# Optimization experiments

Hardware: AMD Instinct MI355X
Metric: run time of the kernel (lower is better)

## Reference

```python
import jax, jax.numpy as jnp
import numpy as np

B, S, D, H = 4, 2048, 1024, 16
DH = D // H  # head dim == module's 'scale'


def setup_inputs() -> dict:
    key = jax.random.key(0)
    ks = jax.random.split(key, 9)
    std = 1.0 / np.sqrt(D)
    return {
        "x": jax.random.normal(ks[0], (B, S, D), dtype=jnp.float32),
        "Wq": jax.random.normal(ks[1], (D, D), dtype=jnp.float32) * std,
        "bq": jax.random.normal(ks[2], (D,), dtype=jnp.float32) * std,
        "Wk": jax.random.normal(ks[3], (D, D), dtype=jnp.float32) * std,
        "bk": jax.random.normal(ks[4], (D,), dtype=jnp.float32) * std,
        "Wv": jax.random.normal(ks[5], (D, D), dtype=jnp.float32) * std,
        "bv": jax.random.normal(ks[6], (D,), dtype=jnp.float32) * std,
        "Wo": jax.random.normal(ks[7], (D, D), dtype=jnp.float32) * std,
        "bo": jax.random.normal(ks[8], (D,), dtype=jnp.float32) * std,
    }


def reference(x, Wq, bq, Wk, bk, Wv, bv, Wo, bo):
    b, s, d = x.shape
    # torch Linear: y = x @ W.T + b
    q = (x @ Wq.T + bq).reshape(b, s, H, DH).transpose(0, 2, 1, 3)  # [B,H,S,Dh]
    k = (x @ Wk.T + bk).reshape(b, s, H, DH).transpose(0, 2, 1, 3)
    v = (x @ Wv.T + bv).reshape(b, s, H, DH).transpose(0, 2, 1, 3)
    # scaled dot-product with causal mask (prefill: Tq == Tk, empty cache)
    scores = jnp.einsum("bhqd,bhkd->bhqk", q, k) / jnp.sqrt(
        jnp.asarray(DH, dtype=jnp.float32))
    causal = jnp.tril(jnp.ones((s, s), dtype=bool))  # [S,S]
    scores = jnp.where(causal, scores, jnp.asarray(-1e9, dtype=scores.dtype))
    attn = jax.nn.softmax(scores, axis=-1)
    out = jnp.einsum("bhqk,bhkd->bhqd", attn, v)  # [B,H,S,Dh]
    out = out.transpose(0, 2, 1, 3).reshape(b, s, d)
    return out @ Wo.T + bo
```

## Files before the change

### kernel.cpp

```cpp
#include <hip/hip_runtime.h>
#include <hip/hip_bf16.h>
#include <stdint.h>

#define NB 4
#define NS 2048
#define ND 1024
#define NH 16
#define NDH 64
#define NM (NB*NS)

typedef __attribute__((ext_vector_type(8))) short bf16x8;
typedef __attribute__((ext_vector_type(4))) float f32x4;
typedef __attribute__((ext_vector_type(16))) float f32x16;
typedef __attribute__((ext_vector_type(8))) unsigned short u16x8;

static __device__ __forceinline__ unsigned short f2bf(float f) {
  union { float f; unsigned u; } v; v.f = f;
  return (unsigned short)((v.u + 0x7FFFu + ((v.u >> 16) & 1u)) >> 16);
}

static __device__ __forceinline__ void gload_lds16(const void* g, void* l) {
  __builtin_amdgcn_global_load_lds(
      (__attribute__((address_space(1))) unsigned int*)(uintptr_t)g,
      (__attribute__((address_space(3))) unsigned int*)(uintptr_t)(size_t)(l),
      16, 0, 0);
}

static __device__ __forceinline__ unsigned cvtpk(float lo, float hi) {
  unsigned r;
  asm("v_cvt_pk_bf16_f32 %0, %1, %2" : "=v"(r) : "v"(lo), "v"(hi));
  return r;
}
static __device__ __forceinline__ void plswap(unsigned &a, unsigned &b) {
  asm("v_permlane32_swap_b32 %0, %1" : "+v"(a), "+v"(b));
}

__global__ void k_cvt(const float* __restrict__ src, unsigned short* __restrict__ dst, int n8) {
  int i = blockIdx.x * blockDim.x + threadIdx.x;
  if (i >= n8) return;
  const float4* s = (const float4*)src + (size_t)i * 2;
  float4 a = s[0], b = s[1];
  u16x8 o;
  o[0]=f2bf(a.x); o[1]=f2bf(a.y); o[2]=f2bf(a.z); o[3]=f2bf(a.w);
  o[4]=f2bf(b.x); o[5]=f2bf(b.y); o[6]=f2bf(b.z); o[7]=f2bf(b.w);
  *((u16x8*)dst + i) = o;
}

__global__ void k_cvtw(const float* __restrict__ s0, const float* __restrict__ s1,
                       const float* __restrict__ s2, const float* __restrict__ s3,
                       unsigned short* __restrict__ d0, unsigned short* __restrict__ d1,
                       unsigned short* __restrict__ d2, unsigned short* __restrict__ d3) {
  constexpr int NG = ND*ND/8;
  int i = blockIdx.x * blockDim.x + threadIdx.x;
  const int m = i / NG, j = i - m*NG;
  const float* src = m==0 ? s0 : (m==1 ? s1 : (m==2 ? s2 : s3));
  unsigned short* dst = m==0 ? d0 : (m==1 ? d1 : (m==2 ? d2 : d3));
  const float4* s = (const float4*)src + (size_t)j * 2;
  float4 a = s[0], b = s[1];
  u16x8 o;
  o[0]=f2bf(a.x); o[1]=f2bf(a.y); o[2]=f2bf(a.z); o[3]=f2bf(a.w);
  o[4]=f2bf(b.x); o[5]=f2bf(b.y); o[6]=f2bf(b.z); o[7]=f2bf(b.w);
  *((u16x8*)dst + j) = o;
}

__global__ __launch_bounds__(256)
void k_gemm_qkv(const unsigned short* __restrict__ A,
                const unsigned short* __restrict__ Wqp, const unsigned short* __restrict__ Wkp,
                const unsigned short* __restrict__ Wvp,
                const float* __restrict__ bqp, const float* __restrict__ bkp,
                const float* __restrict__ bvp,
                unsigned short* __restrict__ Qo, unsigned short* __restrict__ Ko,
                unsigned short* __restrict__ Vto, float qscale)
{
  constexpr int K = ND, BK = 32;
  __shared__ unsigned short Alds[2][128*BK];
  __shared__ unsigned short Blds[2][128*BK];
  const int bcf = blockIdx.x;
  const int mat = bcf >> 3, bc = bcf & 7;
  const unsigned short* W = mat==0 ? Wqp : (mat==1 ? Wkp : Wvp);
  const float* bias = mat==0 ? bqp : (mat==1 ? bkp : bvp);
  const float scale = mat==0 ? qscale : 1.0f;

  const int tid = threadIdx.x;
  const int wid = tid >> 6, lane = tid & 63;
  const int g = lane >> 4, lr = lane & 15;
  const int br = blockIdx.y;
  const int wr = (wid >> 1) << 6, wc = (wid & 1) << 6;

  f32x4 acc[4][4];
  #pragma unroll
  for (int m=0;m<4;m++)
    #pragma unroll
    for (int n=0;n<4;n++) acc[m][n] = f32x4{0.f,0.f,0.f,0.f};

  const unsigned short* Ab = A + (size_t)br*128*K;
  const unsigned short* Wb = W + (size_t)bc*128*K;
  const int r0 = tid >> 2, c0 = (tid & 3) * 8;
  const int r1 = (256 + tid) >> 2;

  auto stage = [&](int b, int k0) {
    gload_lds16(Ab + (size_t)r0*K + k0 + c0, &Alds[b][tid*8]);
    gload_lds16(Ab + (size_t)r1*K + k0 + c0, &Alds[b][(256+tid)*8]);
    gload_lds16(Wb + (size_t)r0*K + k0 + c0, &Blds[b][tid*8]);
    gload_lds16(Wb + (size_t)r1*K + k0 + c0, &Blds[b][(256+tid)*8]);
  };

  stage(0, 0);
  __syncthreads();
  int cur = 0;
  for (int k0 = 0; k0 < K; k0 += BK) {
    if (k0 + BK < K) stage(cur ^ 1, k0 + BK);
    bf16x8 af[4], bfr[4];
    #pragma unroll
    for (int m=0;m<4;m++) af[m]  = *(const bf16x8*)&Alds[cur][(wr + m*16 + lr)*BK + g*8];
    #pragma unroll
    for (int n=0;n<4;n++) bfr[n] = *(const bf16x8*)&Blds[cur][(wc + n*16 + lr)*BK + g*8];
    __builtin_amdgcn_s_setprio(1);
    #pragma unroll
    for (int m=0;m<4;m++)
      #pragma unroll
      for (int n=0;n<4;n++)
        acc[m][n] = __builtin_amdgcn_mfma_f32_16x16x32_bf16(af[m], bfr[n], acc[m][n], 0, 0, 0);
    __builtin_amdgcn_s_setprio(0);
    __syncthreads();
    cur ^= 1;
  }

  #pragma unroll
  for (int m=0;m<4;m++) {
    const int rbase = br*128 + wr + m*16 + g*4;
    #pragma unroll
    for (int n=0;n<4;n++) {
      const int col = bc*128 + wc + n*16 + lr;
      const float bv = bias[col];
      #pragma unroll
      for (int j=0;j<4;j++) {
        const int row = rbase + j;
        const float val = (acc[m][n][j] + bv) * scale;
        const int b = row >> 11, s = row & (NS-1), h = col >> 6, dh = col & 63;
        if (mat == 2)
          Vto[(((size_t)b*NH + h)*NDH + dh)*NS + s] = f2bf(val);
        else
          (mat==0 ? Qo : Ko)[(((size_t)b*NH + h)*NS + s)*NDH + dh] = f2bf(val);
      }
    }
  }
}

__global__ __launch_bounds__(256)
void k_gemm_o(const unsigned short* __restrict__ A,
              const unsigned short* __restrict__ W,
              const float* __restrict__ bias,
              float* __restrict__ outp)
{
  constexpr int K = ND, BK = 32;
  __shared__ unsigned short Alds[2][128*BK];
  __shared__ unsigned short Blds[2][128*BK];
  const int tid = threadIdx.x;
  const int wid = tid >> 6, lane = tid & 63;
  const int g = lane >> 4, lr = lane & 15;
  const int bc = blockIdx.x, br = blockIdx.y;
  const int wr = (wid >> 1) << 6, wc = (wid & 1) << 6;

  f32x4 acc[4][4];
  #pragma unroll
  for (int m=0;m<4;m++)
    #pragma unroll
    for (int n=0;n<4;n++) acc[m][n] = f32x4{0.f,0.f,0.f,0.f};

  const unsigned short* Ab = A + (size_t)br*128*K;
  const unsigned short* Wb = W + (size_t)bc*128*K;
  const int r0 = tid >> 2, c0 = (tid & 3) * 8;
  const int r1 = (256 + tid) >> 2;

  auto stage = [&](int b, int k0) {
    gload_lds16(Ab + (size_t)r0*K + k0 + c0, &Alds[b][tid*8]);
    gload_lds16(Ab + (size_t)r1*K + k0 + c0, &Alds[b][(256+tid)*8]);
    gload_lds16(Wb + (size_t)r0*K + k0 + c0, &Blds[b][tid*8]);
    gload_lds16(Wb + (size_t)r1*K + k0 + c0, &Blds[b][(256+tid)*8]);
  };

  stage(0, 0);
  __syncthreads();
  int cur = 0;
  for (int k0 = 0; k0 < K; k0 += BK) {
    if (k0 + BK < K) stage(cur ^ 1, k0 + BK);
    bf16x8 af[4], bfr[4];
    #pragma unroll
    for (int m=0;m<4;m++) af[m]  = *(const bf16x8*)&Alds[cur][(wr + m*16 + lr)*BK + g*8];
    #pragma unroll
    for (int n=0;n<4;n++) bfr[n] = *(const bf16x8*)&Blds[cur][(wc + n*16 + lr)*BK + g*8];
    __builtin_amdgcn_s_setprio(1);
    #pragma unroll
    for (int m=0;m<4;m++)
      #pragma unroll
      for (int n=0;n<4;n++)
        acc[m][n] = __builtin_amdgcn_mfma_f32_16x16x32_bf16(af[m], bfr[n], acc[m][n], 0, 0, 0);
    __builtin_amdgcn_s_setprio(0);
    __syncthreads();
    cur ^= 1;
  }

  #pragma unroll
  for (int m=0;m<4;m++) {
    const int rbase = br*128 + wr + m*16 + g*4;
    #pragma unroll
    for (int n=0;n<4;n++) {
      const int col = bc*128 + wc + n*16 + lr;
      const float bv = bias[col];
      #pragma unroll
      for (int j=0;j<4;j++)
        outp[(size_t)(rbase + j)*ND + col] = acc[m][n][j] + bv;
    }
  }
}

__global__ __launch_bounds__(128, 4)
void k_attn(const unsigned short* __restrict__ Qg,
            const unsigned short* __restrict__ Kg,
            const unsigned short* __restrict__ Vtg,
            unsigned short* __restrict__ Og)
{
  __shared__ unsigned short Klds[2][64*64];
  __shared__ unsigned short Vlds[2][64*64];
  __shared__ float scL[64];
  const int tid = threadIdx.x;
  const int wid = tid >> 6, lane = tid & 63;
  const int ql = lane & 31, hi = lane >> 5;
  const int bh = blockIdx.x;
  const int qt = (int)gridDim.y - 1 - (int)blockIdx.y;
  const int qbB = qt * 64;
  const int wq = qbB + wid * 32;

  const unsigned short* Qh  = Qg  + (size_t)bh*NS*NDH;
  const unsigned short* Kh  = Kg  + (size_t)bh*NS*NDH;
  const unsigned short* Vth = Vtg + (size_t)bh*NDH*NS;

  bf16x8 qf[4];
  #pragma unroll
  for (int ds=0; ds<4; ++ds)
    qf[ds] = *(const bf16x8*)(Qh + (size_t)(wq+ql)*NDH + ds*16 + hi*8);

  f32x16 acc0, acc1;
  #pragma unroll
  for (int r=0;r<16;++r) { acc0[r]=0.f; acc1[r]=0.f; }
  float lsum = 0.f;

  const int sr = tid >> 3, sc = tid & 7;
  const int swz = (sc ^ (sr & 7)) * 8;

  auto stageKV = [&](int b, int kbase) {
    #pragma unroll
    for (int c=0;c<4;c++)
      gload_lds16(Kh + (size_t)(kbase + c*16 + sr)*NDH + swz, &Klds[b][(c*128+tid)*8]);
    #pragma unroll
    for (int c=0;c<4;c++)
      gload_lds16(Vth + (size_t)(c*16 + sr)*NS + kbase + swz, &Vlds[b][(c*128+tid)*8]);
  };

  const int ntiles = qt + 1;
  stageKV(0, 0);
  __syncthreads();
  int cur = 0;
  for (int kt = 0; kt < ntiles; ++kt) {
    const int kbase = kt << 6;
    if (kt + 1 < ntiles) stageKV(cur ^ 1, (kt+1) << 6);
    #pragma unroll
    for (int h32 = 0; h32 < 2; ++h32) {
      const int kb32 = kbase + h32*32;
      if (kb32 <= wq) {
        const int krow = h32*32 + ql;
        f32x16 st;
        #pragma unroll
        for (int r=0;r<16;++r) st[r] = 0.f;
        __builtin_amdgcn_s_setprio(1);
        #pragma unroll
        for (int ds=0; ds<4; ++ds) {
          bf16x8 kf = *(const bf16x8*)&Klds[cur][krow*64 + (((ds*2+hi) ^ (krow&7))*8)];
          st = __builtin_amdgcn_mfma_f32_32x32x16_bf16(kf, qf[ds], st, 0,0,0);
        }
        __builtin_amdgcn_s_setprio(0);
        if (kb32 == wq) {
          #pragma unroll
          for (int r=0;r<16;++r) {
            const int koff = (r&3) + 8*(r>>2) + 4*hi;
            if (koff > ql) st[r] = -1e30f;
          }
        }
        float p[16]; float ls = 0.f;
        #pragma unroll
        for (int r=0;r<16;++r) { p[r] = __builtin_amdgcn_exp2f(st[r]); ls += p[r]; }
        lsum += ls;
        unsigned w0 = cvtpk(p[0],p[1]),  w1 = cvtpk(p[2],p[3]);
        unsigned w2 = cvtpk(p[4],p[5]),  w3 = cvtpk(p[6],p[7]);
        plswap(w0, w2); plswap(w1, w3);
        unsigned z0 = cvtpk(p[8],p[9]),  z1 = cvtpk(p[10],p[11]);
        unsigned z2 = cvtpk(p[12],p[13]),z3 = cvtpk(p[14],p[15]);
        plswap(z0, z2); plswap(z1, z3);
        union { unsigned u[4]; bf16x8 v; } pk0, pk1;
        pk0.u[0]=w0; pk0.u[1]=w1; pk0.u[2]=w2; pk0.u[3]=w3;
        pk1.u[0]=z0; pk1.u[1]=z1; pk1.u[2]=z2; pk1.u[3]=z3;
        __builtin_amdgcn_s_setprio(1);
        #pragma unroll
        for (int nt=0; nt<2; ++nt) {
          const int drow = nt*32 + ql;
          #pragma unroll
          for (int ksl=0; ksl<2; ++ksl) {
            const int slot = h32*4 + ksl*2 + hi;
            bf16x8 vf = *(const bf16x8*)&Vlds[cur][drow*64 + ((slot ^ (drow&7))*8)];
            f32x16 &a = nt ? acc1 : acc0;
            a = __builtin_amdgcn_mfma_f32_32x32x16_bf16(ksl ? pk1.v : pk0.v, vf, a, 0,0,0);
          }
        }
        __builtin_amdgcn_s_setprio(0);
      }
    }
    __syncthreads();
    cur ^= 1;
  }

  const float l = lsum + __shfl_xor(lsum, 32, 64);
  scL[wid*32 + ql] = 1.0f / l;
  const int b = bh >> 4, h = bh & 15;
  #pragma unroll
  for (int rq=0; rq<4; ++rq) {
    f32x4 lv = *(const f32x4*)&scL[wid*32 + rq*8 + 4*hi];
    #pragma unroll
    for (int j=0;j<4;j++) {
      const float inv = lv[j];
      const int s = wq + rq*8 + 4*hi + j;
      unsigned short* orow = Og + ((size_t)b*NS + s)*ND + h*NDH;
      orow[ql]      = f2bf(acc0[rq*4+j] * inv);
      orow[32 + ql] = f2bf(acc1[rq*4+j] * inv);
    }
  }
}

extern "C" void kernel_launch(void* const* d_in, const int* in_sizes, int n_in,
                              void* d_out, int out_size, void* d_ws, size_t ws_size,
                              hipStream_t stream) {
  (void)in_sizes; (void)n_in; (void)out_size; (void)ws_size;
  const float* x  = (const float*)d_in[0];
  const float* Wq = (const float*)d_in[1];
  const float* bq = (const float*)d_in[2];
  const float* Wk = (const float*)d_in[3];
  const float* bk = (const float*)d_in[4];
  const float* Wv = (const float*)d_in[5];
  const float* bv = (const float*)d_in[6];
  const float* Wo = (const float*)d_in[7];
  const float* bo = (const float*)d_in[8];

  char* ws = (char*)d_ws;
  unsigned short* xb  = (unsigned short*)(ws + 0);
  unsigned short* Wqb = (unsigned short*)(ws + 16777216);
  unsigned short* Wkb = (unsigned short*)(ws + 18874368);
  unsigned short* Wvb = (unsigned short*)(ws + 20971520);
  unsigned short* Wob = (unsigned short*)(ws + 23068672);
  unsigned short* Qb  = (unsigned short*)(ws + 25165824);
  unsigned short* Kb  = (unsigned short*)(ws + 41943040);
  unsigned short* Vtb = (unsigned short*)(ws + 58720256);
  unsigned short* Ob  = (unsigned short*)(ws + 75497472);

  k_cvt<<<dim3(NM*ND/8/256), dim3(256), 0, stream>>>(x, xb, NM*ND/8);
  k_cvtw<<<dim3(4*ND*ND/8/256), dim3(256), 0, stream>>>(Wq, Wk, Wv, Wo, Wqb, Wkb, Wvb, Wob);

  const float qscale = 0.125f * 1.4426950408889634f;
  k_gemm_qkv<<<dim3(24, NM/128), dim3(256), 0, stream>>>(
      xb, Wqb, Wkb, Wvb, bq, bk, bv, Qb, Kb, Vtb, qscale);

  k_attn<<<dim3(NB*NH, NS/64), dim3(128), 0, stream>>>(Qb, Kb, Vtb, Ob);

  k_gemm_o<<<dim3(ND/128, NM/128), dim3(256), 0, stream>>>(Ob, Wob, bo, (float*)d_out);
}
```

Before: 190.2 us.

## Use 256x256 tiles with 8 waves and phased load/MFMA interleaving in QKV GEMM

Rewrites the QKV projection GEMM to use 256x256 output tiles with 512 threads (8 waves, each 128x64). The main loop is split into four phases, with the next tile's global-to-LDS loads interleaved between MFMA groups and explicit waitcnt/barrier control. Larger tiles raise arithmetic intensity, and the fine-grained scheduling is meant to hide load latency. The cost is more LDS (64KB), higher register pressure, and a smaller grid (384 blocks), which may hurt occupancy or tail balance.

```diff
diff --git a/kernel.cpp b/kernel.cpp
--- a/kernel.cpp
+++ b/kernel.cpp
@@ -63,81 +63,103 @@
   *((u16x8*)dst + j) = o;
 }
 
-__global__ __launch_bounds__(256)
-void k_gemm_qkv(const unsigned short* __restrict__ A,
-                const unsigned short* __restrict__ Wqp, const unsigned short* __restrict__ Wkp,
-                const unsigned short* __restrict__ Wvp,
-                const float* __restrict__ bqp, const float* __restrict__ bkp,
-                const float* __restrict__ bvp,
-                unsigned short* __restrict__ Qo, unsigned short* __restrict__ Ko,
-                unsigned short* __restrict__ Vto, float qscale)
+__global__ __launch_bounds__(512, 2)
+void k_gemm_qkv8(const unsigned short* __restrict__ A,
+                 const unsigned short* __restrict__ Wqp, const unsigned short* __restrict__ Wkp,
+                 const unsigned short* __restrict__ Wvp,
+                 const float* __restrict__ bqp, const float* __restrict__ bkp,
+                 const float* __restrict__ bvp,
+                 unsigned short* __restrict__ Qo, unsigned short* __restrict__ Ko,
+                 unsigned short* __restrict__ Vto, float qscale)
 {
-  constexpr int K = ND, BK = 32;
-  __shared__ unsigned short Alds[2][128*BK];
-  __shared__ unsigned short Blds[2][128*BK];
-  const int bcf = blockIdx.x;
-  const int mat = bcf >> 3, bc = bcf & 7;
+  constexpr int K = ND, BK = 32, NT = K / BK;
+  __shared__ unsigned short Al[2][256*BK];
+  __shared__ unsigned short Bl[2][256*BK];
+  const int tid = threadIdx.x;
+  const int lane = tid & 63, wid = tid >> 6;
+  const int g = lane >> 4, lr = lane & 15;
+  const int wr = wid >> 2, wc = wid & 3;
+  const int bc = blockIdx.x, br = blockIdx.y;
+  const int mat = bc >> 2;
   const unsigned short* W = mat==0 ? Wqp : (mat==1 ? Wkp : Wvp);
   const float* bias = mat==0 ? bqp : (mat==1 ? bkp : bvp);
   const float scale = mat==0 ? qscale : 1.0f;
 
-  const int tid = threadIdx.x;
-  const int wid = tid >> 6, lane = tid & 63;
-  const int g = lane >> 4, lr = lane & 15;
-  const int br = blockIdx.y;
-  const int wr = (wid >> 1) << 6, wc = (wid & 1) << 6;
-
-  f32x4 acc[4][4];
-  #pragma unroll
-  for (int m=0;m<4;m++)
+  const unsigned short* Ab = A + (size_t)br*256*K;
+  const unsigned short* Wb = W + (size_t)(bc & 3)*256*K;
+
+  f32x4 acc[8][4];
+  #pragma unroll
+  for (int m=0;m<8;m++)
     #pragma unroll
     for (int n=0;n<4;n++) acc[m][n] = f32x4{0.f,0.f,0.f,0.f};
 
-  const unsigned short* Ab = A + (size_t)br*128*K;
-  const unsigned short* Wb = W + (size_t)bc*128*K;
-  const int r0 = tid >> 2, c0 = (tid & 3) * 8;
-  const int r1 = (256 + tid) >> 2;
-
-  auto stage = [&](int b, int k0) {
-    gload_lds16(Ab + (size_t)r0*K + k0 + c0, &Alds[b][tid*8]);
-    gload_lds16(Ab + (size_t)r1*K + k0 + c0, &Alds[b][(256+tid)*8]);
-    gload_lds16(Wb + (size_t)r0*K + k0 + c0, &Blds[b][tid*8]);
-    gload_lds16(Wb + (size_t)r1*K + k0 + c0, &Blds[b][(256+tid)*8]);
+  const int st_r = tid >> 2;
+  const int st_c = (tid & 3) * 8;
+  auto stageA = [&](int buf, int half, int t) {
+    const int tc = t < NT ? t : NT-1;
+    gload_lds16(Ab + (size_t)(half*128 + st_r)*K + tc*BK + st_c,
+                &Al[buf][half*4096 + tid*8]);
   };
-
-  stage(0, 0);
-  __syncthreads();
-  int cur = 0;
-  for (int k0 = 0; k0 < K; k0 += BK) {
-    if (k0 + BK < K) stage(cur ^ 1, k0 + BK);
-    bf16x8 af[4], bfr[4];
-    #pragma unroll
-    for (int m=0;m<4;m++) af[m]  = *(const bf16x8*)&Alds[cur][(wr + m*16 + lr)*BK + g*8];
-    #pragma unroll
-    for (int n=0;n<4;n++) bfr[n] = *(const bf16x8*)&Blds[cur][(wc + n*16 + lr)*BK + g*8];
-    __builtin_amdgcn_s_setprio(1);
-    #pragma unroll
-    for (int m=0;m<4;m++)
-      #pragma unroll
-      for (int n=0;n<4;n++)
-        acc[m][n] = __builtin_amdgcn_mfma_f32_16x16x32_bf16(af[m], bfr[n], acc[m][n], 0, 0, 0);
-    __builtin_amdgcn_s_setprio(0);
-    __syncthreads();
-    cur ^= 1;
-  }
-
-  #pragma unroll
-  for (int m=0;m<4;m++) {
-    const int rbase = br*128 + wr + m*16 + g*4;
+  auto stageB = [&](int buf, int half, int t) {
+    const int tc = t < NT ? t : NT-1;
+    gload_lds16(Wb + (size_t)(half*128 + st_r)*K + tc*BK + st_c,
+                &Bl[buf][half*4096 + tid*8]);
+  };
+
+#define QKV_PHASE(P, STAGE, VM) do {                                           \
+    bf16x8 af0 = *(const bf16x8*)&Al[cur][(wr*128 + (P)*32 +  0 + lr)*BK + g*8]; \
+    bf16x8 af1 = *(const bf16x8*)&Al[cur][(wr*128 + (P)*32 + 16 + lr)*BK + g*8]; \
+    STAGE;                                                                     \
+    VM;                                                                        \
+    __builtin_amdgcn_s_barrier();                                              \
+    asm volatile("s_waitcnt lgkmcnt(0)" ::: "memory");                         \
+    __builtin_amdgcn_sched_barrier(0);                                         \
+    __builtin_amdgcn_s_setprio(1);                                             \
+    _Pragma("unroll")                                                          \
+    for (int n=0;n<4;n++) {                                                    \
+      acc[(P)*2+0][n] = __builtin_amdgcn_mfma_f32_16x16x32_bf16(af0, bfr[n], acc[(P)*2+0][n],0,0,0); \
+      acc[(P)*2+1][n] = __builtin_amdgcn_mfma_f32_16x16x32_bf16(af1, bfr[n], acc[(P)*2+1][n],0,0,0); \
+    }                                                                          \
+    __builtin_amdgcn_s_setprio(0);                                             \
+  } while(0)
+
+#define QKV_VMW do { asm volatile("s_waitcnt vmcnt(1)" ::: "memory");          \
+                     __builtin_amdgcn_sched_barrier(0); } while(0)
+
+  stageB(0, 0, 0); stageB(0, 1, 0); stageA(0, 0, 0); stageA(0, 1, 0);
+  stageB(1, 0, 1);
+  QKV_VMW;
+  __builtin_amdgcn_s_barrier();
+
+  for (int u = 0; u < NT; ++u) {
+    const int cur = u & 1;
+    bf16x8 bfr[4];
+    #pragma unroll
+    for (int n=0;n<4;n++)
+      bfr[n] = *(const bf16x8*)&Bl[cur][(wc*64 + n*16 + lr)*BK + g*8];
+    QKV_PHASE(0, stageB(cur^1, 1, u+1), );
+    QKV_PHASE(1, stageA(cur^1, 0, u+1), );
+    QKV_PHASE(2, stageA(cur^1, 1, u+1), );
+    QKV_PHASE(3, stageB(cur,   0, u+2), QKV_VMW);
+    __builtin_amdgcn_s_barrier();
+  }
+#undef QKV_PHASE
+#undef QKV_VMW
+
+  #pragma unroll
+  for (int m=0;m<8;m++) {
+    const int rbase = br*256 + wr*128 + m*16 + g*4;
     #pragma unroll
     for (int n=0;n<4;n++) {
-      const int col = bc*128 + wc + n*16 + lr;
-      const float bv = bias[col];
+      const int colm = (bc & 3)*256 + wc*64 + n*16 + lr;
+      const float bv = bias[colm];
+      const int h = colm >> 6, dh = colm & 63;
       #pragma unroll
       for (int j=0;j<4;j++) {
         const int row = rbase + j;
         const float val = (acc[m][n][j] + bv) * scale;
-        const int b = row >> 11, s = row & (NS-1), h = col >> 6, dh = col & 63;
+        const int b = row >> 11, s = row & (NS-1);
         if (mat == 2)
           Vto[(((size_t)b*NH + h)*NDH + dh)*NS + s] = f2bf(val);
         else
@@ -365,7 +387,7 @@
   k_cvtw<<<dim3(4*ND*ND/8/256), dim3(256), 0, stream>>>(Wq, Wk, Wv, Wo, Wqb, Wkb, Wvb, Wob);
 
   const float qscale = 0.125f * 1.4426950408889634f;
-  k_gemm_qkv<<<dim3(24, NM/128), dim3(256), 0, stream>>>(
+  k_gemm_qkv8<<<dim3(12, NM/256), dim3(512), 0, stream>>>(
       xb, Wqb, Wkb, Wvb, bq, bk, bv, Qb, Kb, Vtb, qscale);
 
   k_attn<<<dim3(NB*NH, NS/64), dim3(128), 0, stream>>>(Qb, Kb, Vtb, Ob);
```

Measured after the change: 193.5 us. No clear change (+1.7%).
